# Optimization experiments

Measured on AMD Instinct MI355X. Metric: run time of the kernel, lower is better.

## Reference

```python
import jax, jax.numpy as jnp
import numpy as np
import math

HIDDEN = 4096
N_HEADS = 32
N_KV_HEADS = 8
HEAD_DIM = HIDDEN // N_HEADS  # 128
N_GROUPS = N_HEADS // N_KV_HEADS  # 4
ROPE_THETA = 10000.0


def setup_inputs() -> dict:
    key = jax.random.key(0)
    ks = jax.random.split(key, 5)
    B, S = 2, 2048
    hidden_states = jax.random.normal(ks[0], (B, S, HIDDEN), dtype=jnp.float32)
    position_ids = jnp.broadcast_to(jnp.arange(S, dtype=jnp.int32)[None, :], (B, S))
    sc = 1.0 / math.sqrt(HIDDEN)
    Wq = jax.random.normal(ks[1], (HIDDEN, N_HEADS * HEAD_DIM), dtype=jnp.float32) * sc
    Wk = jax.random.normal(ks[2], (HIDDEN, N_KV_HEADS * HEAD_DIM), dtype=jnp.float32) * sc
    Wv = jax.random.normal(ks[3], (HIDDEN, N_KV_HEADS * HEAD_DIM), dtype=jnp.float32) * sc
    Wo = jax.random.normal(ks[4], (HIDDEN, HIDDEN), dtype=jnp.float32) * sc
    return {"hidden_states": hidden_states, "position_ids": position_ids,
            "Wq": Wq, "Wk": Wk, "Wv": Wv, "Wo": Wo}


def _rope_cos_sin(position_ids):
    # inv_freq: [head_dim//2]
    inv_freq = 1.0 / (ROPE_THETA ** (jnp.arange(0, HEAD_DIM, 2, dtype=jnp.float32) / HEAD_DIM))
    freqs = position_ids.astype(jnp.float32)[..., None] * inv_freq  # [B, S, hd/2]
    emb = jnp.concatenate([freqs, freqs], axis=-1)  # [B, S, hd]
    return jnp.cos(emb), jnp.sin(emb)


def _rotate_half(x):
    h = x.shape[-1] // 2
    return jnp.concatenate([-x[..., h:], x[..., :h]], axis=-1)


def _apply_rope(x, cos, sin):
    # x: [B, H, S, hd]; cos/sin: [B, S, hd] -> unsqueeze head dim
    return x * cos[:, None] + _rotate_half(x) * sin[:, None]


def reference(hidden_states, position_ids, Wq, Wk, Wv, Wo):
    B, S, _ = hidden_states.shape
    q = (hidden_states @ Wq).reshape(B, S, N_HEADS, HEAD_DIM).transpose(0, 2, 1, 3)
    k = (hidden_states @ Wk).reshape(B, S, N_KV_HEADS, HEAD_DIM).transpose(0, 2, 1, 3)
    v = (hidden_states @ Wv).reshape(B, S, N_KV_HEADS, HEAD_DIM).transpose(0, 2, 1, 3)

    cos, sin = _rope_cos_sin(position_ids)
    q = _apply_rope(q, cos, sin)
    k = _apply_rope(k, cos, sin)

    # repeat_kv: (B, kvH, S, d) -> (B, H, S, d)
    k = jnp.repeat(k, N_GROUPS, axis=1)
    v = jnp.repeat(v, N_GROUPS, axis=1)

    scores = jnp.einsum('bhqd,bhkd->bhqk', q, k) / math.sqrt(HEAD_DIM)
    causal = jnp.tril(jnp.ones((S, S), dtype=bool))
    neg = jnp.finfo(jnp.float32).min
    scores = jnp.where(causal[None, None], scores, neg)
    attn = jax.nn.softmax(scores.astype(jnp.float32), axis=-1).astype(q.dtype)

    out = jnp.einsum('bhqk,bhkd->bhqd', attn, v)
    out = out.transpose(0, 2, 1, 3).reshape(B, S, HIDDEN)
    return out @ Wo
```

## Files before the change

kernel.cpp:

```cpp
#include <hip/hip_runtime.h>
#include <hip/hip_bf16.h>
#include <math.h>

#define HIDDEN 4096
#define NH 32
#define NKV 8
#define HD 128
#define S_LEN 2048
#define BATCH 2
#define MROWS (BATCH * S_LEN)
#define QKVW 6144

typedef __attribute__((ext_vector_type(8))) __bf16 bf16x8;
typedef __attribute__((ext_vector_type(4))) float f32x4;

__device__ __forceinline__ f32x4 mfma16(bf16x8 a, bf16x8 b, f32x4 c) {
  return __builtin_amdgcn_mfma_f32_16x16x32_bf16(a, b, c, 0, 0, 0);
}

__device__ __forceinline__ void gload16(const __bf16* g, const __bf16* l) {
  __builtin_amdgcn_global_load_lds(
      (const __attribute__((address_space(1))) void*)g,
      (__attribute__((address_space(3))) void*)l, 16, 0, 0);
}

#define SBAR()                          \
  do {                                  \
    __builtin_amdgcn_sched_barrier(0);  \
    __builtin_amdgcn_s_barrier();       \
    __builtin_amdgcn_sched_barrier(0);  \
  } while (0)

__global__ __launch_bounds__(256) void cvt_kernel(const float* __restrict__ in,
                                                  __bf16* __restrict__ out, int n) {
  int i = (blockIdx.x * 256 + threadIdx.x) * 8;
  if (i >= n) return;
  float4 a = *reinterpret_cast<const float4*>(in + i);
  float4 b = *reinterpret_cast<const float4*>(in + i + 4);
  bf16x8 t;
  t[0] = (__bf16)a.x; t[1] = (__bf16)a.y; t[2] = (__bf16)a.z; t[3] = (__bf16)a.w;
  t[4] = (__bf16)b.x; t[5] = (__bf16)b.y; t[6] = (__bf16)b.z; t[7] = (__bf16)b.w;
  *reinterpret_cast<bf16x8*>(out + i) = t;
}

__global__ __launch_bounds__(256) void tcvt3_kernel(const float* __restrict__ Wq,
                                                    const float* __restrict__ Wk,
                                                    const float* __restrict__ Wv,
                                                    __bf16* __restrict__ Wt) {
  __shared__ float t[32][33];
  int z = blockIdx.z;
  const float* in;
  __bf16* out;
  int C;
  if (z == 0)      { in = Wq; out = Wt;                         C = 4096; }
  else if (z == 1) { in = Wk; out = Wt + (size_t)4096 * 4096;   C = 1024; }
  else             { in = Wv; out = Wt + (size_t)5120 * 4096;   C = 1024; }
  if ((int)blockIdx.x * 32 >= C) return;
  int tx = threadIdx.x, ty = threadIdx.y;
  int r0 = blockIdx.y * 32, c0 = blockIdx.x * 32;
#pragma unroll
  for (int i = 0; i < 4; i++)
    t[ty + i * 8][tx] = in[(size_t)(r0 + ty + i * 8) * C + c0 + tx];
  __syncthreads();
#pragma unroll
  for (int i = 0; i < 4; i++)
    out[(size_t)(c0 + ty + i * 8) * 4096 + r0 + tx] = (__bf16)t[tx][ty + i * 8];
}

__global__ __launch_bounds__(256) void tcvt_f32(const float* __restrict__ in,
                                                __bf16* __restrict__ out,
                                                int R, int C) {
  __shared__ float t[32][33];
  int tx = threadIdx.x, ty = threadIdx.y;
  int r0 = blockIdx.y * 32, c0 = blockIdx.x * 32;
#pragma unroll
  for (int i = 0; i < 4; i++)
    t[ty + i * 8][tx] = in[(size_t)(r0 + ty + i * 8) * C + c0 + tx];
  __syncthreads();
#pragma unroll
  for (int i = 0; i < 4; i++)
    out[(size_t)(c0 + ty + i * 8) * R + r0 + tx] = (__bf16)t[tx][ty + i * 8];
}

__global__ __launch_bounds__(256) void tvt_kernel(const __bf16* __restrict__ qkv,
                                                  __bf16* __restrict__ vt) {
  __shared__ __bf16 t[32][33];
  int tx = threadIdx.x, ty = threadIdx.y;
  int z = blockIdx.z;
  int b = z >> 3, kvh = z & 7;
  int kv0 = blockIdx.y * 32, d0 = blockIdx.x * 32;
#pragma unroll
  for (int i = 0; i < 4; i++)
    t[ty + i * 8][tx] =
        qkv[(size_t)(b * S_LEN + kv0 + ty + i * 8) * QKVW + 5120 + kvh * HD + d0 + tx];
  __syncthreads();
#pragma unroll
  for (int i = 0; i < 4; i++)
    vt[((size_t)z * HD + d0 + ty + i * 8) * S_LEN + kv0 + tx] = t[tx][ty + i * 8];
}

template<typename CT>
__global__ __launch_bounds__(512, 2) void gemm256(const __bf16* __restrict__ A,
                                                  const __bf16* __restrict__ Bt,
                                                  CT* __restrict__ C,
                                                  int K, int ldc, int nbx) {
  __shared__ char lds[131072];
  const int tid = threadIdx.x;
  const int l = tid & 63, w = tid >> 6;
  const int lrow = l & 15, lg = l >> 4;
  const int sw = (lrow & 7) << 4;

  int nwg = gridDim.x;
  int swz = (blockIdx.x & 7) * (nwg >> 3) + (blockIdx.x >> 3);
  int bx = swz % nbx, by = swz / nbx;
  int m0 = by * 256, n0 = bx * 256;

  const int rA = w * 8 + (l >> 3);
  const int csw = ((l & 7) ^ (l >> 3)) * 8;
  const __bf16* As_[2][2];
  const __bf16* Bs_[2][2];
#pragma unroll
  for (int h = 0; h < 2; h++)
#pragma unroll
    for (int p = 0; p < 2; p++) {
      As_[h][p] = A + (size_t)(m0 + h * 128 + p * 64 + rA) * K + csw;
      Bs_[h][p] = Bt + (size_t)(n0 + h * 128 + p * 64 + rA) * K + csw;
    }

  auto stageA = [&](int par, int h, int kt) {
#pragma unroll
    for (int p = 0; p < 2; p++)
      gload16(As_[h][p] + kt * 64,
              (const __bf16*)(lds + par * 32768 + h * 16384 + p * 8192 + w * 1024));
  };
  auto stageB = [&](int par, int h, int kt) {
#pragma unroll
    for (int p = 0; p < 2; p++)
      gload16(Bs_[h][p] + kt * 64,
              (const __bf16*)(lds + 65536 + par * 32768 + h * 16384 + p * 8192 + w * 1024));
  };

  const int arbase = (w >> 2) * 64 + lrow;
  const int brbase = (w & 3) * 32 + lrow;

  bf16x8 aA[4][2];
  bf16x8 bB[2][2][2];

  auto readA = [&](int par, int ah) {
#pragma unroll
    for (int i = 0; i < 4; i++)
#pragma unroll
      for (int kk = 0; kk < 2; kk++)
        aA[i][kk] = *reinterpret_cast<const bf16x8*>(
            lds + par * 32768 + (arbase + i * 16 + ah * 128) * 128 +
            ((kk * 64 + lg * 16) ^ sw));
  };
  auto readB = [&](int par, int bh) {
#pragma unroll
    for (int j = 0; j < 2; j++)
#pragma unroll
      for (int kk = 0; kk < 2; kk++)
        bB[bh][j][kk] = *reinterpret_cast<const bf16x8*>(
            lds + 65536 + par * 32768 + (brbase + j * 16 + bh * 128) * 128 +
            ((kk * 64 + lg * 16) ^ sw));
  };

  f32x4 acc[8][4];
#pragma unroll
  for (int i = 0; i < 8; i++)
#pragma unroll
    for (int j = 0; j < 4; j++) {
      acc[i][j][0] = 0.f; acc[i][j][1] = 0.f; acc[i][j][2] = 0.f; acc[i][j][3] = 0.f;
    }

  const int NT = K >> 6;

  stageA(0, 0, 0); stageA(0, 1, 0); stageB(0, 0, 0); stageB(0, 1, 0);
  stageA(1, 0, 1); stageB(1, 0, 1);
  __builtin_amdgcn_sched_barrier(0);
  asm volatile("s_waitcnt vmcnt(4)" ::: "memory");
  SBAR();

  for (int t = 0; t < NT; t++) {
    const int par = t & 1, npar = par ^ 1;
    const int t1 = (t + 1 < NT) ? t + 1 : 0;
    const int t2 = (t + 2 < NT) ? t + 2 : 0;

#define MFMA_QUAD(AH, BH)                                                   \
  __builtin_amdgcn_s_setprio(1);                                            \
  _Pragma("unroll") for (int i4 = 0; i4 < 4; i4++)                          \
      _Pragma("unroll") for (int j2 = 0; j2 < 2; j2++)                      \
          _Pragma("unroll") for (int kk = 0; kk < 2; kk++)                  \
              acc[(AH)*4 + i4][(BH)*2 + j2] =                               \
                  mfma16(aA[i4][kk], bB[BH][j2][kk], acc[(AH)*4 + i4][(BH)*2 + j2]); \
  __builtin_amdgcn_s_setprio(0);

    readA(par, 0);
    readB(par, 0);
    stageA(npar, 1, t1);
    SBAR();
    MFMA_QUAD(0, 0);
    SBAR();
    readB(par, 1);
    stageB(npar, 1, t1);
    SBAR();
    MFMA_QUAD(0, 1);
    SBAR();
    readA(par, 1);
    stageA(par, 0, t2);
    SBAR();
    MFMA_QUAD(1, 0);
    SBAR();
    stageB(par, 0, t2);
    SBAR();
    MFMA_QUAD(1, 1);
    __builtin_amdgcn_sched_barrier(0);
    asm volatile("s_waitcnt vmcnt(4)" ::: "memory");
    SBAR();
#undef MFMA_QUAD
  }

#pragma unroll
  for (int i = 0; i < 8; i++) {
    int row = m0 + (w >> 2) * 64 + (i & 3) * 16 + (i >> 2) * 128 + lg * 4;
#pragma unroll
    for (int j = 0; j < 4; j++) {
      int col = n0 + (w & 3) * 32 + (j & 1) * 16 + (j >> 1) * 128 + lrow;
#pragma unroll
      for (int jj = 0; jj < 4; jj++)
        C[(size_t)(row + jj) * ldc + col] = (CT)acc[i][j][jj];
    }
  }
}

template<typename CT>
__global__ __launch_bounds__(512, 2) void gemm128(const __bf16* __restrict__ A,
                                                  const __bf16* __restrict__ Bt,
                                                  CT* __restrict__ C,
                                                  int K, int ldc, int nbx) {
  __shared__ char lds[98304];
  const int tid = threadIdx.x;
  const int l = tid & 63, w = tid >> 6;
  const int lrow = l & 15, lg = l >> 4;
  const int sw = (lrow & 7) << 4;

  int nwg = gridDim.x;
  int swz = (blockIdx.x & 7) * (nwg >> 3) + (blockIdx.x >> 3);
  int bx = swz % nbx, by = swz / nbx;
  int m0 = by * 256, n0 = bx * 128;

  const int rA = w * 8 + (l >> 3);
  const int csw = ((l & 7) ^ (l >> 3)) * 8;
  const __bf16* As_[2][2];
  const __bf16* Bs_[2];
#pragma unroll
  for (int h = 0; h < 2; h++)
#pragma unroll
    for (int p = 0; p < 2; p++)
      As_[h][p] = A + (size_t)(m0 + h * 128 + p * 64 + rA) * K + csw;
#pragma unroll
  for (int p = 0; p < 2; p++)
    Bs_[p] = Bt + (size_t)(n0 + p * 64 + rA) * K + csw;

  auto stageA = [&](int par, int h, int kt) {
#pragma unroll
    for (int p = 0; p < 2; p++)
      gload16(As_[h][p] + kt * 64,
              (const __bf16*)(lds + par * 32768 + h * 16384 + p * 8192 + w * 1024));
  };
  auto stageB = [&](int par, int kt) {
#pragma unroll
    for (int p = 0; p < 2; p++)
      gload16(Bs_[p] + kt * 64,
              (const __bf16*)(lds + 65536 + par * 16384 + p * 8192 + w * 1024));
  };

  const int arbase = (w >> 2) * 64 + lrow;
  const int brbase = (w & 3) * 32 + lrow;

  bf16x8 aA[4][2];
  bf16x8 bB[2][2];

  auto readA = [&](int par, int ah) {
#pragma unroll
    for (int i = 0; i < 4; i++)
#pragma unroll
      for (int kk = 0; kk < 2; kk++)
        aA[i][kk] = *reinterpret_cast<const bf16x8*>(
            lds + par * 32768 + (arbase + i * 16 + ah * 128) * 128 +
            ((kk * 64 + lg * 16) ^ sw));
  };
  auto readB = [&](int par) {
#pragma unroll
    for (int j = 0; j < 2; j++)
#pragma unroll
      for (int kk = 0; kk < 2; kk++)
        bB[j][kk] = *reinterpret_cast<const bf16x8*>(
            lds + 65536 + par * 16384 + (brbase + j * 16) * 128 +
            ((kk * 64 + lg * 16) ^ sw));
  };

  f32x4 acc[8][2];
#pragma unroll
  for (int i = 0; i < 8; i++)
#pragma unroll
    for (int j = 0; j < 2; j++) {
      acc[i][j][0] = 0.f; acc[i][j][1] = 0.f; acc[i][j][2] = 0.f; acc[i][j][3] = 0.f;
    }

  const int NT = K >> 6;

  stageA(0, 0, 0); stageA(0, 1, 0); stageB(0, 0);
  stageA(1, 0, 1);
  __builtin_amdgcn_sched_barrier(0);
  asm volatile("s_waitcnt vmcnt(2)" ::: "memory");
  SBAR();

  for (int t = 0; t < NT; t++) {
    const int par = t & 1, npar = par ^ 1;
    const int t1 = (t + 1 < NT) ? t + 1 : 0;
    const int t2 = (t + 2 < NT) ? t + 2 : 0;

#define MFMA_HALF(AH)                                                        \
  __builtin_amdgcn_s_setprio(1);                                             \
  _Pragma("unroll") for (int i4 = 0; i4 < 4; i4++)                           \
      _Pragma("unroll") for (int j2 = 0; j2 < 2; j2++)                       \
          _Pragma("unroll") for (int kk = 0; kk < 2; kk++)                   \
              acc[(AH)*4 + i4][j2] =                                         \
                  mfma16(aA[i4][kk], bB[j2][kk], acc[(AH)*4 + i4][j2]);      \
  __builtin_amdgcn_s_setprio(0);

    readA(par, 0);
    readB(par);
    stageA(npar, 1, t1);
    stageB(npar, t1);
    SBAR();
    MFMA_HALF(0);
    SBAR();
    readA(par, 1);
    stageA(par, 0, t2);
    SBAR();
    MFMA_HALF(1);
    __builtin_amdgcn_sched_barrier(0);
    asm volatile("s_waitcnt vmcnt(2)" ::: "memory");
    SBAR();
#undef MFMA_HALF
  }

#pragma unroll
  for (int i = 0; i < 8; i++) {
    int row = m0 + (w >> 2) * 64 + (i & 3) * 16 + (i >> 2) * 128 + lg * 4;
#pragma unroll
    for (int j = 0; j < 2; j++) {
      int col = n0 + (w & 3) * 32 + j * 16 + lrow;
#pragma unroll
      for (int jj = 0; jj < 4; jj++)
        C[(size_t)(row + jj) * ldc + col] = (CT)acc[i][j][jj];
    }
  }
}

__global__ __launch_bounds__(256) void rope_kernel(__bf16* __restrict__ qkv,
                                                   const int* __restrict__ pos) {
  int row = blockIdx.x;
  int t = threadIdx.x;
  float p = (float)pos[row];
  __bf16* rbase = qkv + (size_t)row * QKVW;

  {
    int head = t >> 3, chunk = t & 7;
    __bf16* base = rbase + head * HD + chunk * 8;
    bf16x8 x1 = *reinterpret_cast<const bf16x8*>(base);
    bf16x8 x2 = *reinterpret_cast<const bf16x8*>(base + 64);
    bf16x8 o1, o2;
#pragma unroll
    for (int e = 0; e < 8; e++) {
      float ang = p * exp2f(-0.20762050f * (float)(chunk * 8 + e));
      float s, c;
      __sincosf(ang, &s, &c);
      float a = (float)x1[e], b2 = (float)x2[e];
      o1[e] = (__bf16)(a * c - b2 * s);
      o2[e] = (__bf16)(b2 * c + a * s);
    }
    *reinterpret_cast<bf16x8*>(base) = o1;
    *reinterpret_cast<bf16x8*>(base + 64) = o2;
  }
  if (t < 64) {
    int head = t >> 3, chunk = t & 7;
    __bf16* base = rbase + 4096 + head * HD + chunk * 8;
    bf16x8 x1 = *reinterpret_cast<const bf16x8*>(base);
    bf16x8 x2 = *reinterpret_cast<const bf16x8*>(base + 64);
    bf16x8 o1, o2;
#pragma unroll
    for (int e = 0; e < 8; e++) {
      float ang = p * exp2f(-0.20762050f * (float)(chunk * 8 + e));
      float s, c;
      __sincosf(ang, &s, &c);
      float a = (float)x1[e], b2 = (float)x2[e];
      o1[e] = (__bf16)(a * c - b2 * s);
      o2[e] = (__bf16)(b2 * c + a * s);
    }
    *reinterpret_cast<bf16x8*>(base) = o1;
    *reinterpret_cast<bf16x8*>(base + 64) = o2;
  }
}

__global__ __launch_bounds__(512) void attn_kernel(const __bf16* __restrict__ qkv,
                                                   const __bf16* __restrict__ vt,
                                                   __bf16* __restrict__ out) {
  __shared__ __bf16 Ks[64 * 128];
  __shared__ __bf16 Vs[128 * 64];
  __shared__ __bf16 Ps[8][32][68];

  int tid = threadIdx.x;
  int l = tid & 63, w = tid >> 6;
  int bid = blockIdx.x;
  int qblk = 7 - (bid >> 6);
  int rem = bid & 63;
  int h = rem & 31, b = rem >> 5;
  int kvh = h >> 2;
  int q0w = qblk * 256 + w * 32;
  int lrow = l & 15, lg = l >> 4;
  int sw = (lrow & 7) << 4;
  const float SCL = 0.08838834764831845f * 1.4426950408889634f;

  const __bf16* kbase = qkv + (size_t)(b * S_LEN) * QKVW + 4096 + kvh * HD;
  const __bf16* vbase = vt + ((size_t)(b * NKV + kvh) * HD) * S_LEN;

  int krow = tid >> 3;
  int kslot = (tid & 7) * 2;
  int vrow = tid >> 2;
  int vslot = (tid & 3) * 2;
  char* KsB = (char*)Ks;
  char* VsB = (char*)Vs;
  int koff0 = krow * 256 + ((kslot * 16) ^ ((krow & 7) << 4));
  int koff1 = krow * 256 + (((kslot + 1) * 16) ^ ((krow & 7) << 4));
  int voff0 = vrow * 128 + ((vslot * 16) ^ ((vrow & 7) << 4));
  int voff1 = vrow * 128 + (((vslot + 1) * 16) ^ ((vrow & 7) << 4));
  const __bf16* kg = kbase + (size_t)krow * QKVW + kslot * 8;
  const __bf16* vg = vbase + (size_t)vrow * S_LEN + vslot * 8;

  bf16x8 qf[2][4];
#pragma unroll
  for (int mi = 0; mi < 2; mi++) {
    const __bf16* qp = qkv + (size_t)(b * S_LEN + q0w + mi * 16 + lrow) * QKVW + h * HD + lg * 8;
#pragma unroll
    for (int kk = 0; kk < 4; kk++) {
      bf16x8 t = *reinterpret_cast<const bf16x8*>(qp + kk * 32);
#pragma unroll
      for (int e = 0; e < 8; e++) t[e] = (__bf16)((float)t[e] * SCL);
      qf[mi][kk] = t;
    }
  }

  f32x4 ov[2][8];
#pragma unroll
  for (int mi = 0; mi < 2; mi++)
#pragma unroll
    for (int n = 0; n < 8; n++) {
      ov[mi][n][0] = 0.f; ov[mi][n][1] = 0.f; ov[mi][n][2] = 0.f; ov[mi][n][3] = 0.f;
    }
  float m[2][4], ssum[2][4];
#pragma unroll
  for (int mi = 0; mi < 2; mi++)
#pragma unroll
    for (int jj = 0; jj < 4; jj++) { m[mi][jj] = -3.0e38f; ssum[mi][jj] = 0.f; }

  int nt = 4 * qblk + 4;
  bf16x8 kr0, kr1, vr0, vr1;

  kr0 = *reinterpret_cast<const bf16x8*>(kg);
  kr1 = *reinterpret_cast<const bf16x8*>(kg + 8);
  vr0 = *reinterpret_cast<const bf16x8*>(vg);
  vr1 = *reinterpret_cast<const bf16x8*>(vg + 8);
  *reinterpret_cast<bf16x8*>(KsB + koff0) = kr0;
  *reinterpret_cast<bf16x8*>(KsB + koff1) = kr1;
  *reinterpret_cast<bf16x8*>(VsB + voff0) = vr0;
  *reinterpret_cast<bf16x8*>(VsB + voff1) = vr1;
  __syncthreads();

  for (int t = 0;; t++) {
    int kv0 = t * 64;
    bool more = (t + 1 < nt);
    if (more) {
      int kvn = kv0 + 64;
      kr0 = *reinterpret_cast<const bf16x8*>(kg + (size_t)kvn * QKVW);
      kr1 = *reinterpret_cast<const bf16x8*>(kg + (size_t)kvn * QKVW + 8);
      vr0 = *reinterpret_cast<const bf16x8*>(vg + kvn);
      vr1 = *reinterpret_cast<const bf16x8*>(vg + kvn + 8);
    }

    bool active = (kv0 <= q0w + 31);
    if (active) {
      f32x4 sc[2][4];
#pragma unroll
      for (int mi = 0; mi < 2; mi++)
#pragma unroll
        for (int c = 0; c < 4; c++) {
          sc[mi][c][0] = 0.f; sc[mi][c][1] = 0.f; sc[mi][c][2] = 0.f; sc[mi][c][3] = 0.f;
        }
#pragma unroll
      for (int c = 0; c < 4; c++) {
        int rb = (c * 16 + lrow) * 256;
#pragma unroll
        for (int kk = 0; kk < 4; kk++) {
          bf16x8 kf = *reinterpret_cast<const bf16x8*>(KsB + rb + ((kk * 64 + lg * 16) ^ sw));
          sc[0][c] = mfma16(qf[0][kk], kf, sc[0][c]);
          sc[1][c] = mfma16(qf[1][kk], kf, sc[1][c]);
        }
      }

      bool bound = (kv0 + 64 > q0w);
      if (bound) {
#pragma unroll
        for (int mi = 0; mi < 2; mi++)
#pragma unroll
          for (int jj = 0; jj < 4; jj++) {
            int qidx = q0w + mi * 16 + lg * 4 + jj;
            if (kv0 + lrow > qidx)      sc[mi][0][jj] = -3.0e38f;
            if (kv0 + 16 + lrow > qidx) sc[mi][1][jj] = -3.0e38f;
            if (kv0 + 32 + lrow > qidx) sc[mi][2][jj] = -3.0e38f;
            if (kv0 + 48 + lrow > qidx) sc[mi][3][jj] = -3.0e38f;
          }
      }

      float lm[2][4];
      bool lanegrow = false;
#pragma unroll
      for (int mi = 0; mi < 2; mi++)
#pragma unroll
        for (int jj = 0; jj < 4; jj++) {
          lm[mi][jj] = fmaxf(fmaxf(sc[mi][0][jj], sc[mi][1][jj]),
                             fmaxf(sc[mi][2][jj], sc[mi][3][jj]));
          lanegrow |= (lm[mi][jj] > m[mi][jj] + 8.0f);
        }

      if (__any(lanegrow)) {
        float es[2][4];
#pragma unroll
        for (int mi = 0; mi < 2; mi++)
#pragma unroll
          for (int jj = 0; jj < 4; jj++) {
            float r = lm[mi][jj];
            r = fmaxf(r, __shfl_xor(r, 1));
            r = fmaxf(r, __shfl_xor(r, 2));
            r = fmaxf(r, __shfl_xor(r, 4));
            r = fmaxf(r, __shfl_xor(r, 8));
            float mo = m[mi][jj];
            bool grow = (r > mo + 8.0f);
            float mn = grow ? r : mo;
            float e = grow ? exp2f(mo - r) : 1.0f;
            es[mi][jj] = e;
            m[mi][jj] = mn;
            ssum[mi][jj] *= e;
          }
#pragma unroll
        for (int mi = 0; mi < 2; mi++)
#pragma unroll
          for (int n = 0; n < 8; n++)
#pragma unroll
            for (int jj = 0; jj < 4; jj++) ov[mi][n][jj] *= es[mi][jj];
      }

#pragma unroll
      for (int mi = 0; mi < 2; mi++)
#pragma unroll
        for (int jj = 0; jj < 4; jj++) {
          float mn = m[mi][jj];
          float p0 = exp2f(sc[mi][0][jj] - mn), p1 = exp2f(sc[mi][1][jj] - mn);
          float p2 = exp2f(sc[mi][2][jj] - mn), p3 = exp2f(sc[mi][3][jj] - mn);
          ssum[mi][jj] += (p0 + p1) + (p2 + p3);
          int pr = mi * 16 + lg * 4 + jj;
          Ps[w][pr][lrow]      = (__bf16)p0;
          Ps[w][pr][16 + lrow] = (__bf16)p1;
          Ps[w][pr][32 + lrow] = (__bf16)p2;
          Ps[w][pr][48 + lrow] = (__bf16)p3;
        }

#pragma unroll
      for (int kvs = 0; kvs < 2; kvs++) {
        bf16x8 pf0 = *reinterpret_cast<const bf16x8*>(&Ps[w][lrow][kvs * 32 + lg * 8]);
        bf16x8 pf1 = *reinterpret_cast<const bf16x8*>(&Ps[w][16 + lrow][kvs * 32 + lg * 8]);
#pragma unroll
        for (int n = 0; n < 8; n++) {
          bf16x8 vf = *reinterpret_cast<const bf16x8*>(
              VsB + (n * 16 + lrow) * 128 + ((kvs * 64 + lg * 16) ^ sw));
          ov[0][n] = mfma16(pf0, vf, ov[0][n]);
          ov[1][n] = mfma16(pf1, vf, ov[1][n]);
        }
      }
    }

    if (!more) break;
    __syncthreads();
    *reinterpret_cast<bf16x8*>(KsB + koff0) = kr0;
    *reinterpret_cast<bf16x8*>(KsB + koff1) = kr1;
    *reinterpret_cast<bf16x8*>(VsB + voff0) = vr0;
    *reinterpret_cast<bf16x8*>(VsB + voff1) = vr1;
    __syncthreads();
  }

  float rinv[2][4];
#pragma unroll
  for (int mi = 0; mi < 2; mi++)
#pragma unroll
    for (int jj = 0; jj < 4; jj++) {
      float s = ssum[mi][jj];
      s += __shfl_xor(s, 1);
      s += __shfl_xor(s, 2);
      s += __shfl_xor(s, 4);
      s += __shfl_xor(s, 8);
      rinv[mi][jj] = 1.0f / s;
    }
#pragma unroll
  for (int mi = 0; mi < 2; mi++)
#pragma unroll
    for (int n = 0; n < 8; n++)
#pragma unroll
      for (int jj = 0; jj < 4; jj++) {
        out[(size_t)(b * S_LEN + q0w + mi * 16 + lg * 4 + jj) * HIDDEN + h * HD + n * 16 + lrow] =
            (__bf16)(ov[mi][n][jj] * rinv[mi][jj]);
      }
}

extern "C" void kernel_launch(void* const* d_in, const int* in_sizes, int n_in,
                              void* d_out, int out_size, void* d_ws, size_t ws_size,
                              hipStream_t stream) {
  const float* hidden = (const float*)d_in[0];
  const int* posids   = (const int*)d_in[1];
  const float* Wq     = (const float*)d_in[2];
  const float* Wk     = (const float*)d_in[3];
  const float* Wv     = (const float*)d_in[4];
  const float* Wo     = (const float*)d_in[5];
  float* out = (float*)d_out;

  char* ws = (char*)d_ws;
  __bf16* h_bf    = (__bf16*)(ws + 0);
  __bf16* a_buf   = h_bf;
  __bf16* Wt      = (__bf16*)(ws + 33554432);
  __bf16* qkv_buf = (__bf16*)(ws + 83886080);
  __bf16* vt_buf  = (__bf16*)(ws + 134217728);

  dim3 b256(256), b328(32, 8), b512(512);

  cvt_kernel<<<dim3(MROWS * HIDDEN / (256 * 8)), b256, 0, stream>>>(hidden, h_bf, MROWS * HIDDEN);

  tcvt3_kernel<<<dim3(128, 128, 3), b328, 0, stream>>>(Wq, Wk, Wv, Wt);

  gemm256<__bf16><<<dim3(256), b512, 0, stream>>>(
      h_bf, Wt, qkv_buf, HIDDEN, QKVW, 4096 / 256);
  gemm128<__bf16><<<dim3(256), b512, 0, stream>>>(
      h_bf, Wt + (size_t)4096 * 4096, qkv_buf + 4096, HIDDEN, QKVW, 2048 / 128);

  rope_kernel<<<dim3(MROWS), b256, 0, stream>>>(qkv_buf, posids);

  tvt_kernel<<<dim3(HD / 32, S_LEN / 32, BATCH * NKV), b328, 0, stream>>>(qkv_buf, vt_buf);

  attn_kernel<<<dim3(8 * NH * BATCH), b512, 0, stream>>>(qkv_buf, vt_buf, a_buf);

  tcvt_f32<<<dim3(HIDDEN / 32, HIDDEN / 32), b328, 0, stream>>>(Wo, Wt, HIDDEN, HIDDEN);

  gemm256<float><<<dim3(256), b512, 0, stream>>>(
      a_buf, Wt, out, HIDDEN, HIDDEN, HIDDEN / 256);
}
```

Measured before the change: 485.9 us.

## Restructure GEMM prefetch pipeline and pack P stores with permuted V layout

Both GEMM kernels get a reworked software pipeline. The prologue interleaves A/B staging, the main loop is unrolled by two with compile-time buffer parity, and waits use deeper vmcnt thresholds so more global loads stay in flight with fewer barriers per tile. Separately, the attention kernel packs pairs of bf16 P values into 32-bit LDS stores, and the V-transpose kernel permutes key columns so that packed layout still lines up with the PV MFMA. This cuts LDS store instructions, but correctness depends on the permutation matching exactly and on NT being even.

```diff
diff --git a/kernel.cpp b/kernel.cpp
--- a/kernel.cpp
+++ b/kernel.cpp
@@ -29,6 +29,18 @@
     __builtin_amdgcn_sched_barrier(0);  \
     __builtin_amdgcn_s_barrier();       \
     __builtin_amdgcn_sched_barrier(0);  \
+  } while (0)
+
+#define VMCNT8()                                              \
+  do {                                                        \
+    __builtin_amdgcn_sched_barrier(0);                        \
+    asm volatile("s_waitcnt vmcnt(8)" ::: "memory");          \
+  } while (0)
+
+#define VMCNT6()                                              \
+  do {                                                        \
+    __builtin_amdgcn_sched_barrier(0);                        \
+    asm volatile("s_waitcnt vmcnt(6)" ::: "memory");          \
   } while (0)
 
 __global__ __launch_bounds__(256) void cvt_kernel(const float* __restrict__ in,
@@ -94,9 +106,10 @@
     t[ty + i * 8][tx] =
         qkv[(size_t)(b * S_LEN + kv0 + ty + i * 8) * QKVW + 5120 + kvh * HD + d0 + tx];
   __syncthreads();
+  int cperm = kv0 + 2 * (tx & 15) + (tx >> 4);
 #pragma unroll
   for (int i = 0; i < 4; i++)
-    vt[((size_t)z * HD + d0 + ty + i * 8) * S_LEN + kv0 + tx] = t[tx][ty + i * 8];
+    vt[((size_t)z * HD + d0 + ty + i * 8) * S_LEN + cperm] = t[tx][ty + i * 8];
 }
 
 template<typename CT>
@@ -175,16 +188,11 @@
 
   const int NT = K >> 6;
 
-  stageA(0, 0, 0); stageA(0, 1, 0); stageB(0, 0, 0); stageB(0, 1, 0);
+  stageA(0, 0, 0); stageB(0, 0, 0);
+  stageA(0, 1, 0); stageB(0, 1, 0);
   stageA(1, 0, 1); stageB(1, 0, 1);
-  __builtin_amdgcn_sched_barrier(0);
-  asm volatile("s_waitcnt vmcnt(4)" ::: "memory");
+  VMCNT8();
   SBAR();
-
-  for (int t = 0; t < NT; t++) {
-    const int par = t & 1, npar = par ^ 1;
-    const int t1 = (t + 1 < NT) ? t + 1 : 0;
-    const int t2 = (t + 2 < NT) ? t + 2 : 0;
 
 #define MFMA_QUAD(AH, BH)                                                   \
   __builtin_amdgcn_s_setprio(1);                                            \
@@ -195,30 +203,38 @@
                   mfma16(aA[i4][kk], bB[BH][j2][kk], acc[(AH)*4 + i4][(BH)*2 + j2]); \
   __builtin_amdgcn_s_setprio(0);
 
-    readA(par, 0);
-    readB(par, 0);
-    stageA(npar, 1, t1);
-    SBAR();
-    MFMA_QUAD(0, 0);
-    SBAR();
-    readB(par, 1);
-    stageB(npar, 1, t1);
-    SBAR();
-    MFMA_QUAD(0, 1);
-    SBAR();
-    readA(par, 1);
-    stageA(par, 0, t2);
-    SBAR();
-    MFMA_QUAD(1, 0);
-    SBAR();
-    stageB(par, 0, t2);
-    SBAR();
-    MFMA_QUAD(1, 1);
-    __builtin_amdgcn_sched_barrier(0);
-    asm volatile("s_waitcnt vmcnt(4)" ::: "memory");
-    SBAR();
+#define GTILE256(PAR, TT)                                                   \
+  {                                                                         \
+    const int t1n = ((TT) + 1 < NT) ? (TT) + 1 : 0;                         \
+    const int t2n = ((TT) + 2 < NT) ? (TT) + 2 : 0;                         \
+    readA(PAR, 0);                                                          \
+    readB(PAR, 0);                                                          \
+    stageA(PAR ^ 1, 1, t1n);                                                \
+    stageB(PAR ^ 1, 1, t1n);                                                \
+    VMCNT8();                                                               \
+    SBAR();                                                                 \
+    MFMA_QUAD(0, 0);                                                        \
+    SBAR();                                                                 \
+    readB(PAR, 1);                                                          \
+    stageA(PAR, 0, t2n);                                                    \
+    SBAR();                                                                 \
+    MFMA_QUAD(0, 1);                                                        \
+    SBAR();                                                                 \
+    readA(PAR, 1);                                                          \
+    stageB(PAR, 0, t2n);                                                    \
+    SBAR();                                                                 \
+    MFMA_QUAD(1, 0);                                                        \
+    MFMA_QUAD(1, 1);                                                        \
+    VMCNT8();                                                               \
+    SBAR();                                                                 \
+  }
+
+  for (int t = 0; t < NT; t += 2) {
+    GTILE256(0, t);
+    GTILE256(1, t + 1);
+  }
+#undef GTILE256
 #undef MFMA_QUAD
-  }
 
 #pragma unroll
   for (int i = 0; i < 8; i++) {
@@ -310,16 +326,10 @@
 
   const int NT = K >> 6;
 
-  stageA(0, 0, 0); stageA(0, 1, 0); stageB(0, 0);
-  stageA(1, 0, 1);
-  __builtin_amdgcn_sched_barrier(0);
-  asm volatile("s_waitcnt vmcnt(2)" ::: "memory");
+  stageA(0, 0, 0); stageB(0, 0);
+  stageA(0, 1, 0); stageB(1, 1); stageA(1, 0, 1);
+  VMCNT6();
   SBAR();
-
-  for (int t = 0; t < NT; t++) {
-    const int par = t & 1, npar = par ^ 1;
-    const int t1 = (t + 1 < NT) ? t + 1 : 0;
-    const int t2 = (t + 2 < NT) ? t + 2 : 0;
 
 #define MFMA_HALF(AH)                                                        \
   __builtin_amdgcn_s_setprio(1);                                             \
@@ -330,22 +340,32 @@
                   mfma16(aA[i4][kk], bB[j2][kk], acc[(AH)*4 + i4][j2]);      \
   __builtin_amdgcn_s_setprio(0);
 
-    readA(par, 0);
-    readB(par);
-    stageA(npar, 1, t1);
-    stageB(npar, t1);
-    SBAR();
-    MFMA_HALF(0);
-    SBAR();
-    readA(par, 1);
-    stageA(par, 0, t2);
-    SBAR();
-    MFMA_HALF(1);
-    __builtin_amdgcn_sched_barrier(0);
-    asm volatile("s_waitcnt vmcnt(2)" ::: "memory");
-    SBAR();
+#define GTILE128(PAR, TT)                                                    \
+  {                                                                          \
+    const int t1n = ((TT) + 1 < NT) ? (TT) + 1 : 0;                          \
+    const int t2n = ((TT) + 2 < NT) ? (TT) + 2 : 0;                          \
+    readA(PAR, 0);                                                           \
+    readB(PAR);                                                              \
+    stageA(PAR ^ 1, 1, t1n);                                                 \
+    VMCNT6();                                                                \
+    SBAR();                                                                  \
+    MFMA_HALF(0);                                                            \
+    SBAR();                                                                  \
+    readA(PAR, 1);                                                           \
+    stageB(PAR, t2n);                                                        \
+    stageA(PAR, 0, t2n);                                                     \
+    SBAR();                                                                  \
+    MFMA_HALF(1);                                                            \
+    VMCNT6();                                                                \
+    SBAR();                                                                  \
+  }
+
+  for (int t = 0; t < NT; t += 2) {
+    GTILE128(0, t);
+    GTILE128(1, t + 1);
+  }
+#undef GTILE128
 #undef MFMA_HALF
-  }
 
 #pragma unroll
   for (int i = 0; i < 8; i++) {
@@ -571,10 +591,11 @@
           float p2 = exp2f(sc[mi][2][jj] - mn), p3 = exp2f(sc[mi][3][jj] - mn);
           ssum[mi][jj] += (p0 + p1) + (p2 + p3);
           int pr = mi * 16 + lg * 4 + jj;
-          Ps[w][pr][lrow]      = (__bf16)p0;
-          Ps[w][pr][16 + lrow] = (__bf16)p1;
-          Ps[w][pr][32 + lrow] = (__bf16)p2;
-          Ps[w][pr][48 + lrow] = (__bf16)p3;
+          union { __bf16 hh[2]; unsigned int u; } a01, a23;
+          a01.hh[0] = (__bf16)p0; a01.hh[1] = (__bf16)p1;
+          a23.hh[0] = (__bf16)p2; a23.hh[1] = (__bf16)p3;
+          *reinterpret_cast<unsigned int*>(&Ps[w][pr][2 * lrow]) = a01.u;
+          *reinterpret_cast<unsigned int*>(&Ps[w][pr][32 + 2 * lrow]) = a23.u;
         }
 
 #pragma unroll
```

After: 468.2 us. -3.6%, faster.
